# Kernel tuning notes

Hardware: AMD Instinct MI355X
Metric: run time of the kernel (lower is better)

Reference implementation:

```python
import jax, jax.numpy as jnp
import numpy as np

P = 64
K = 64
D = 2048
KERNEL_MUL = 2.0
KERNEL_NUM = 5


def setup_inputs() -> dict:
    key = jax.random.key(0)
    k1, k2 = jax.random.split(key)
    source = jax.random.normal(k1, (P * K, D), dtype=jnp.float32)
    target = jax.random.normal(k2, (P * K, D), dtype=jnp.float32)
    return {"source": source, "target": target}


def _mmd_terms(source, target):
    # split into P groups of K rows each, process all splits at once
    src = source.reshape(P, K, D)
    tgt = target.reshape(P, K, D)
    total = jnp.concatenate([src, tgt], axis=1)          # [P, 2K, D]
    n = 2 * K
    # pairwise squared L2 distances per split: [P, 2K, 2K]
    sq = jnp.sum(total * total, axis=-1)                  # [P, 2K]
    gram = jnp.einsum('pid,pjd->pij', total, total)       # [P, 2K, 2K]
    l2 = sq[:, :, None] + sq[:, None, :] - 2.0 * gram
    # bandwidth from detached distances (torch uses L2_distance.data)
    bw = jax.lax.stop_gradient(jnp.sum(l2, axis=(1, 2))) / (n * n - n)  # [P]
    bw = bw / (KERNEL_MUL ** (KERNEL_NUM // 2))
    mults = KERNEL_MUL ** jnp.arange(KERNEL_NUM, dtype=jnp.float32)     # [kn]
    bws = bw[:, None] * mults[None, :] + 1e-9                           # [P, kn]
    # multi-bandwidth Gaussian kernel sum: [P, 2K, 2K]
    kern = jnp.sum(jnp.exp(-l2[:, None, :, :] / bws[:, :, None, None]), axis=1)
    XX = kern[:, :K, :K]
    YY = kern[:, K:, K:]
    XY = kern[:, :K, K:]
    YX = kern[:, K:, :K]
    xx = jnp.mean(XX, axis=(1, 2))
    yy = jnp.mean(YY, axis=(1, 2))
    xy = jnp.mean(XY, axis=(1, 2))
    yx = jnp.mean(YX, axis=(1, 2))
    per_split_loss = xx + yy - xy - yx                    # [P]
    total_loss = jnp.sum(per_split_loss) / P
    return total_loss, l2, xx, yy, xy, yx


def reference(source, target):
    total_loss, l2, xx, yy, xy, yx = _mmd_terms(source, target)
    # original returns max of l2dist from the LAST split only
    max_l2_last = jnp.max(l2[-1])
    return (total_loss.reshape(1), max_l2_last,
            jnp.sum(xx) / P, jnp.sum(yy) / P, jnp.sum(xy) / P, jnp.sum(yx) / P)
```

## Files before the change

kernel.cpp:

```cpp
#include <hip/hip_runtime.h>

typedef _Float16 half8 __attribute__((ext_vector_type(8)));
typedef float floatx4 __attribute__((ext_vector_type(4)));
typedef unsigned int uint2v __attribute__((ext_vector_type(2)));

#define NSPLIT 64
#define KS 64
#define DIM 2048
#define NROW 128
#define BK 128
#define KSPL 4
#define KCH (DIM / KSPL)
#define NKC_A (KCH / BK)
#define SST 152
#define GSZ (NROW * NROW)
#define NBLK (NSPLIT * KSPL)
#define GT2_OFF (NBLK * GSZ)
#define PART_OFF (GT2_OFF + NBLK)


__device__ __forceinline__ unsigned int pk16(float a, float b) {
  return __builtin_bit_cast(unsigned int, __builtin_amdgcn_cvt_pkrtz(a, b));
}

__global__ __launch_bounds__(1024) void gram_kernel(const float* __restrict__ src,
                                                    const float* __restrict__ tgt,
                                                    float* __restrict__ ws) {
  __shared__ __align__(16) _Float16 stage[NROW * SST];
  __shared__ float red[16];

  const int p = blockIdx.x >> 2;
  const int c = blockIdx.x & (KSPL - 1);
  const int tid = threadIdx.x;
  const int lane = tid & 63;
  const int wave = tid >> 6;

  const int srow = tid >> 3;
  const int c4 = (tid & 7) * 4;
  const float* rowp = ((srow < KS) ? (src + (size_t)(p * KS + srow) * DIM)
                                   : (tgt + (size_t)(p * KS + (srow - KS)) * DIM)) +
                      c * KCH;

  const int wr = (wave >> 2) * 32;
  const int wc = (wave & 3) * 32;
  const int fr = lane & 15;
  const int fk = (lane >> 4) * 8;

  floatx4 acc00 = {0.f, 0.f, 0.f, 0.f};
  floatx4 acc01 = {0.f, 0.f, 0.f, 0.f};
  floatx4 acc10 = {0.f, 0.f, 0.f, 0.f};
  floatx4 acc11 = {0.f, 0.f, 0.f, 0.f};

  float4 f0, f1, f2, f3;
#define LOADK(kc)                                      \
  do {                                                 \
    const float* gp_ = rowp + (kc) * BK + c4;          \
    f0 = *(const float4*)(gp_);                        \
    f1 = *(const float4*)(gp_ + 32);                   \
    f2 = *(const float4*)(gp_ + 64);                   \
    f3 = *(const float4*)(gp_ + 96);                   \
  } while (0)

  LOADK(0);
  for (int kc = 0; kc < NKC_A; ++kc) {
    __syncthreads();
    {
      _Float16* sp = &stage[srow * SST + c4];
      *(uint2v*)(sp)      = (uint2v){pk16(f0.x, f0.y), pk16(f0.z, f0.w)};
      *(uint2v*)(sp + 32) = (uint2v){pk16(f1.x, f1.y), pk16(f1.z, f1.w)};
      *(uint2v*)(sp + 64) = (uint2v){pk16(f2.x, f2.y), pk16(f2.z, f2.w)};
      *(uint2v*)(sp + 96) = (uint2v){pk16(f3.x, f3.y), pk16(f3.z, f3.w)};
    }
    __syncthreads();
    if (kc + 1 < NKC_A) LOADK(kc + 1);
#pragma unroll
    for (int ks = 0; ks < 4; ++ks) {
      const int ko = ks * 32 + fk;
      half8 a0 = *(const half8*)&stage[(wr + fr) * SST + ko];
      half8 a1 = *(const half8*)&stage[(wr + 16 + fr) * SST + ko];
      half8 b0 = *(const half8*)&stage[(wc + fr) * SST + ko];
      half8 b1 = *(const half8*)&stage[(wc + 16 + fr) * SST + ko];
      acc00 = __builtin_amdgcn_mfma_f32_16x16x32_f16(a0, b0, acc00, 0, 0, 0);
      acc01 = __builtin_amdgcn_mfma_f32_16x16x32_f16(a0, b1, acc01, 0, 0, 0);
      acc10 = __builtin_amdgcn_mfma_f32_16x16x32_f16(a1, b0, acc10, 0, 0, 0);
      acc11 = __builtin_amdgcn_mfma_f32_16x16x32_f16(a1, b1, acc11, 0, 0, 0);
    }
  }
#undef LOADK

  float* wsp = ws + (size_t)blockIdx.x * GSZ + wave * 1024 + lane * 4;
  *(floatx4*)(wsp)       = acc00;
  *(floatx4*)(wsp + 256) = acc01;
  *(floatx4*)(wsp + 512) = acc10;
  *(floatx4*)(wsp + 768) = acc11;

  float gsum = 0.0f;
#pragma unroll
  for (int r = 0; r < 4; ++r) gsum += acc00[r] + acc01[r] + acc10[r] + acc11[r];
#pragma unroll
  for (int m = 1; m <= 32; m <<= 1) gsum += __shfl_xor(gsum, m, 64);
  if (lane == 0) red[wave] = gsum;
  __syncthreads();
  if (tid == 0) {
    float t = 0.0f;
    for (int w = 0; w < 16; ++w) t += red[w];
    ws[GT2_OFF + blockIdx.x] = t;
  }
}

__global__ __launch_bounds__(1024) void reduce_kernel(const float* __restrict__ ws,
                                                      float* __restrict__ out) {
  __shared__ float sqv[NROW];
  __shared__ float bcast[8];
  __shared__ float redm[16];
  __shared__ float quad2[2];

  const int b = blockIdx.x;
  const int p = b >> 2;
  const int rb = b & 3;
  const int tid = threadIdx.x;
  const int lane = tid & 63;
  const int wave = tid >> 6;

  const int row = rb * 32 + (tid >> 5);
  const int cg = tid & 31;

  const float* sb = ws + (size_t)(p * KSPL) * GSZ;
  const int wv = ((row >> 5) << 2) + (cg >> 3);
  const int a = (((row >> 4) & 1) << 1) + ((cg >> 2) & 1);
  const int ln = (((row & 15) >> 2) << 4) + ((cg & 3) << 2);
  const int idx = wv * 1024 + a * 256 + ln * 4 + (row & 3);

  float g0 = 0.f, g1 = 0.f, g2 = 0.f, g3 = 0.f;
#pragma unroll
  for (int c8 = 0; c8 < KSPL; ++c8) {
    const float* bp = sb + (size_t)c8 * GSZ + idx;
    g0 += bp[0]; g1 += bp[4]; g2 += bp[8]; g3 += bp[12];
  }

  if (tid < NROW) {
    const int i = tid;
    const int wd = (i >> 5) * 5;
    const int ad = ((i >> 4) & 1) * 3;
    const int lnd = (((i & 15) >> 2) << 4) + (i & 15);
    const int idxd = wd * 1024 + ad * 256 + lnd * 4 + (i & 3);
    float d = 0.0f;
#pragma unroll
    for (int c8 = 0; c8 < KSPL; ++c8) d += sb[(size_t)c8 * GSZ + idxd];
    sqv[i] = d;
  }
  if (tid < 2) quad2[tid] = 0.0f;
  __syncthreads();

  if (tid == 0) {
    float ssq = 0.0f;
    for (int i = 0; i < NROW; ++i) ssq += sqv[i];
    float gt = ws[GT2_OFF + p * 4 + 0] + ws[GT2_OFF + p * 4 + 1] +
               ws[GT2_OFF + p * 4 + 2] + ws[GT2_OFF + p * 4 + 3];
    float suml2 = 2.0f * (float)NROW * ssq - 2.0f * gt;
    float bw = suml2 / (float)(NROW * NROW - NROW) * 0.25f;
    float mult = 1.0f;
    for (int k = 0; k < 5; ++k) {
      bcast[k] = 1.0f / (bw * mult + 1e-9f);
      mult *= 2.0f;
    }
  }
  __syncthreads();

  const float sqi = sqv[row];
  float l2r[4];
  float lmax = 0.0f;
  {
    const float gg[4] = {g0, g1, g2, g3};
#pragma unroll
    for (int k = 0; k < 4; ++k) {
      float v = sqi + sqv[cg * 4 + k] - 2.0f * gg[k];
      l2r[k] = v;
      lmax = fmaxf(lmax, v);
    }
  }
#pragma unroll
  for (int m = 1; m <= 32; m <<= 1) lmax = fmaxf(lmax, __shfl_xor(lmax, m, 64));
  if (lane == 0) redm[wave] = lmax;

  const float ib0 = bcast[0], ib1 = bcast[1], ib2 = bcast[2], ib3 = bcast[3], ib4 = bcast[4];
  float qsum = 0.0f;
#pragma unroll
  for (int k = 0; k < 4; ++k) {
    float v = l2r[k];
    qsum += __expf(-v * ib0) + __expf(-v * ib1) + __expf(-v * ib2) +
            __expf(-v * ib3) + __expf(-v * ib4);
  }
  qsum += __shfl_xor(qsum, 1, 64);
  qsum += __shfl_xor(qsum, 2, 64);
  qsum += __shfl_xor(qsum, 4, 64);
  qsum += __shfl_xor(qsum, 8, 64);
  qsum += __shfl_xor(qsum, 32, 64);
  if (lane == 0) atomicAdd(&quad2[0], qsum);
  if (lane == 16) atomicAdd(&quad2[1], qsum);
  __syncthreads();

  if (tid == 0) {
    float mx = 0.0f;
    for (int w = 0; w < 16; ++w) mx = fmaxf(mx, redm[w]);
    float4* part = (float4*)(ws + PART_OFF);
    part[b] = make_float4(quad2[0], quad2[1], mx, 0.0f);
  }
}

__global__ __launch_bounds__(256) void final_kernel(const float* __restrict__ ws,
                                                    float* __restrict__ out) {
  __shared__ float fr[4][5];
  const int tid = threadIdx.x;
  const int lane = tid & 63;
  const int wave = tid >> 6;
  const float4* part = (const float4*)(ws + PART_OFF);
  float4 pt = part[tid];
  const int rb = tid & 3;
  float xx = (rb < 2) ? pt.x : 0.0f;
  float xy = (rb < 2) ? pt.y : 0.0f;
  float yx = (rb >= 2) ? pt.x : 0.0f;
  float yy = (rb >= 2) ? pt.y : 0.0f;
  float mx = ((tid >> 2) == NSPLIT - 1) ? pt.z : 0.0f;
#pragma unroll
  for (int m = 1; m <= 32; m <<= 1) {
    xx += __shfl_xor(xx, m, 64);
    xy += __shfl_xor(xy, m, 64);
    yx += __shfl_xor(yx, m, 64);
    yy += __shfl_xor(yy, m, 64);
    mx = fmaxf(mx, __shfl_xor(mx, m, 64));
  }
  if (lane == 0) {
    fr[wave][0] = xx; fr[wave][1] = xy; fr[wave][2] = yx; fr[wave][3] = yy; fr[wave][4] = mx;
  }
  __syncthreads();
  if (tid == 0) {
    float sxx = 0, sxy = 0, syx = 0, syy = 0, smx = 0;
    for (int w = 0; w < 4; ++w) {
      sxx += fr[w][0]; sxy += fr[w][1]; syx += fr[w][2]; syy += fr[w][3];
      smx = fmaxf(smx, fr[w][4]);
    }
    const float inv = 1.0f / (4096.0f * 64.0f);
    out[0] = (sxx + syy - sxy - syx) * inv;
    out[1] = smx;
    out[2] = sxx * inv;
    out[3] = syy * inv;
    out[4] = sxy * inv;
    out[5] = syx * inv;
  }
}

extern "C" void kernel_launch(void* const* d_in, const int* in_sizes, int n_in,
                              void* d_out, int out_size, void* d_ws, size_t ws_size,
                              hipStream_t stream) {
  const float* src = (const float*)d_in[0];
  const float* tgt = (const float*)d_in[1];
  float* out = (float*)d_out;
  float* ws = (float*)d_ws;
  gram_kernel<<<NBLK, 1024, 0, stream>>>(src, tgt, ws);
  reduce_kernel<<<NBLK, 1024, 0, stream>>>(ws, out);
  final_kernel<<<1, 256, 0, stream>>>(ws, out);
}
```

Baseline: 109.5 us.

## Fuse gram, reduce and final kernels into one cooperative kernel with grid syncs

Merges the three kernel launches into a single cooperative kernel that uses grid-wide syncs between the gram, per-split reduction and final reduction phases. This removes two kernel launch boundaries and their gaps. The cost is grid.sync overhead and a requirement that all 256 blocks of 1024 threads be co-resident. If they are not, the cooperative launch fails.

```diff
diff --git a/kernel.cpp b/kernel.cpp
--- a/kernel.cpp
+++ b/kernel.cpp
@@ -1,4 +1,7 @@
 #include <hip/hip_runtime.h>
+#include <hip/hip_cooperative_groups.h>
+
+namespace cg = cooperative_groups;
 
 typedef _Float16 half8 __attribute__((ext_vector_type(8)));
 typedef float floatx4 __attribute__((ext_vector_type(4)));
@@ -23,230 +26,231 @@
   return __builtin_bit_cast(unsigned int, __builtin_amdgcn_cvt_pkrtz(a, b));
 }
 
-__global__ __launch_bounds__(1024) void gram_kernel(const float* __restrict__ src,
-                                                    const float* __restrict__ tgt,
-                                                    float* __restrict__ ws) {
+__global__ __launch_bounds__(1024) void mmd_fused(const float* __restrict__ src,
+                                                  const float* __restrict__ tgt,
+                                                  float* __restrict__ ws,
+                                                  float* __restrict__ out) {
   __shared__ __align__(16) _Float16 stage[NROW * SST];
   __shared__ float red[16];
-
-  const int p = blockIdx.x >> 2;
-  const int c = blockIdx.x & (KSPL - 1);
-  const int tid = threadIdx.x;
-  const int lane = tid & 63;
-  const int wave = tid >> 6;
-
-  const int srow = tid >> 3;
-  const int c4 = (tid & 7) * 4;
-  const float* rowp = ((srow < KS) ? (src + (size_t)(p * KS + srow) * DIM)
-                                   : (tgt + (size_t)(p * KS + (srow - KS)) * DIM)) +
-                      c * KCH;
-
-  const int wr = (wave >> 2) * 32;
-  const int wc = (wave & 3) * 32;
-  const int fr = lane & 15;
-  const int fk = (lane >> 4) * 8;
-
-  floatx4 acc00 = {0.f, 0.f, 0.f, 0.f};
-  floatx4 acc01 = {0.f, 0.f, 0.f, 0.f};
-  floatx4 acc10 = {0.f, 0.f, 0.f, 0.f};
-  floatx4 acc11 = {0.f, 0.f, 0.f, 0.f};
-
-  float4 f0, f1, f2, f3;
-#define LOADK(kc)                                      \
-  do {                                                 \
-    const float* gp_ = rowp + (kc) * BK + c4;          \
-    f0 = *(const float4*)(gp_);                        \
-    f1 = *(const float4*)(gp_ + 32);                   \
-    f2 = *(const float4*)(gp_ + 64);                   \
-    f3 = *(const float4*)(gp_ + 96);                   \
-  } while (0)
-
-  LOADK(0);
-  for (int kc = 0; kc < NKC_A; ++kc) {
-    __syncthreads();
-    {
-      _Float16* sp = &stage[srow * SST + c4];
-      *(uint2v*)(sp)      = (uint2v){pk16(f0.x, f0.y), pk16(f0.z, f0.w)};
-      *(uint2v*)(sp + 32) = (uint2v){pk16(f1.x, f1.y), pk16(f1.z, f1.w)};
-      *(uint2v*)(sp + 64) = (uint2v){pk16(f2.x, f2.y), pk16(f2.z, f2.w)};
-      *(uint2v*)(sp + 96) = (uint2v){pk16(f3.x, f3.y), pk16(f3.z, f3.w)};
-    }
-    __syncthreads();
-    if (kc + 1 < NKC_A) LOADK(kc + 1);
-#pragma unroll
-    for (int ks = 0; ks < 4; ++ks) {
-      const int ko = ks * 32 + fk;
-      half8 a0 = *(const half8*)&stage[(wr + fr) * SST + ko];
-      half8 a1 = *(const half8*)&stage[(wr + 16 + fr) * SST + ko];
-      half8 b0 = *(const half8*)&stage[(wc + fr) * SST + ko];
-      half8 b1 = *(const half8*)&stage[(wc + 16 + fr) * SST + ko];
-      acc00 = __builtin_amdgcn_mfma_f32_16x16x32_f16(a0, b0, acc00, 0, 0, 0);
-      acc01 = __builtin_amdgcn_mfma_f32_16x16x32_f16(a0, b1, acc01, 0, 0, 0);
-      acc10 = __builtin_amdgcn_mfma_f32_16x16x32_f16(a1, b0, acc10, 0, 0, 0);
-      acc11 = __builtin_amdgcn_mfma_f32_16x16x32_f16(a1, b1, acc11, 0, 0, 0);
-    }
-  }
-#undef LOADK
-
-  float* wsp = ws + (size_t)blockIdx.x * GSZ + wave * 1024 + lane * 4;
-  *(floatx4*)(wsp)       = acc00;
-  *(floatx4*)(wsp + 256) = acc01;
-  *(floatx4*)(wsp + 512) = acc10;
-  *(floatx4*)(wsp + 768) = acc11;
-
-  float gsum = 0.0f;
-#pragma unroll
-  for (int r = 0; r < 4; ++r) gsum += acc00[r] + acc01[r] + acc10[r] + acc11[r];
-#pragma unroll
-  for (int m = 1; m <= 32; m <<= 1) gsum += __shfl_xor(gsum, m, 64);
-  if (lane == 0) red[wave] = gsum;
-  __syncthreads();
-  if (tid == 0) {
-    float t = 0.0f;
-    for (int w = 0; w < 16; ++w) t += red[w];
-    ws[GT2_OFF + blockIdx.x] = t;
-  }
-}
-
-__global__ __launch_bounds__(1024) void reduce_kernel(const float* __restrict__ ws,
-                                                      float* __restrict__ out) {
   __shared__ float sqv[NROW];
   __shared__ float bcast[8];
   __shared__ float redm[16];
   __shared__ float quad2[2];
+  __shared__ float fr[4][5];
+
+  cg::grid_group grid = cg::this_grid();
 
   const int b = blockIdx.x;
   const int p = b >> 2;
-  const int rb = b & 3;
+  const int c = b & (KSPL - 1);
   const int tid = threadIdx.x;
   const int lane = tid & 63;
   const int wave = tid >> 6;
 
-  const int row = rb * 32 + (tid >> 5);
-  const int cg = tid & 31;
-
-  const float* sb = ws + (size_t)(p * KSPL) * GSZ;
-  const int wv = ((row >> 5) << 2) + (cg >> 3);
-  const int a = (((row >> 4) & 1) << 1) + ((cg >> 2) & 1);
-  const int ln = (((row & 15) >> 2) << 4) + ((cg & 3) << 2);
-  const int idx = wv * 1024 + a * 256 + ln * 4 + (row & 3);
-
-  float g0 = 0.f, g1 = 0.f, g2 = 0.f, g3 = 0.f;
-#pragma unroll
-  for (int c8 = 0; c8 < KSPL; ++c8) {
-    const float* bp = sb + (size_t)c8 * GSZ + idx;
-    g0 += bp[0]; g1 += bp[4]; g2 += bp[8]; g3 += bp[12];
+  {
+    const int srow = tid >> 3;
+    const int c4 = (tid & 7) * 4;
+    const float* rowp = ((srow < KS) ? (src + (size_t)(p * KS + srow) * DIM)
+                                     : (tgt + (size_t)(p * KS + (srow - KS)) * DIM)) +
+                        c * KCH;
+
+    const int wr = (wave >> 2) * 32;
+    const int wc = (wave & 3) * 32;
+    const int frr = lane & 15;
+    const int fk = (lane >> 4) * 8;
+
+    floatx4 acc00 = {0.f, 0.f, 0.f, 0.f};
+    floatx4 acc01 = {0.f, 0.f, 0.f, 0.f};
+    floatx4 acc10 = {0.f, 0.f, 0.f, 0.f};
+    floatx4 acc11 = {0.f, 0.f, 0.f, 0.f};
+
+    float4 f0, f1, f2, f3;
+#define LOADK(kc)                                      \
+    do {                                               \
+      const float* gp_ = rowp + (kc) * BK + c4;        \
+      f0 = *(const float4*)(gp_);                      \
+      f1 = *(const float4*)(gp_ + 32);                 \
+      f2 = *(const float4*)(gp_ + 64);                 \
+      f3 = *(const float4*)(gp_ + 96);                 \
+    } while (0)
+
+    LOADK(0);
+    for (int kc = 0; kc < NKC_A; ++kc) {
+      __syncthreads();
+      {
+        _Float16* sp = &stage[srow * SST + c4];
+        *(uint2v*)(sp)      = (uint2v){pk16(f0.x, f0.y), pk16(f0.z, f0.w)};
+        *(uint2v*)(sp + 32) = (uint2v){pk16(f1.x, f1.y), pk16(f1.z, f1.w)};
+        *(uint2v*)(sp + 64) = (uint2v){pk16(f2.x, f2.y), pk16(f2.z, f2.w)};
+        *(uint2v*)(sp + 96) = (uint2v){pk16(f3.x, f3.y), pk16(f3.z, f3.w)};
+      }
+      __syncthreads();
+      if (kc + 1 < NKC_A) LOADK(kc + 1);
+#pragma unroll
+      for (int ks = 0; ks < 4; ++ks) {
+        const int ko = ks * 32 + fk;
+        half8 a0 = *(const half8*)&stage[(wr + frr) * SST + ko];
+        half8 a1 = *(const half8*)&stage[(wr + 16 + frr) * SST + ko];
+        half8 b0 = *(const half8*)&stage[(wc + frr) * SST + ko];
+        half8 b1 = *(const half8*)&stage[(wc + 16 + frr) * SST + ko];
+        acc00 = __builtin_amdgcn_mfma_f32_16x16x32_f16(a0, b0, acc00, 0, 0, 0);
+        acc01 = __builtin_amdgcn_mfma_f32_16x16x32_f16(a0, b1, acc01, 0, 0, 0);
+        acc10 = __builtin_amdgcn_mfma_f32_16x16x32_f16(a1, b0, acc10, 0, 0, 0);
+        acc11 = __builtin_amdgcn_mfma_f32_16x16x32_f16(a1, b1, acc11, 0, 0, 0);
+      }
+    }
+#undef LOADK
+
+    float* wsp = ws + (size_t)b * GSZ + wave * 1024 + lane * 4;
+    *(floatx4*)(wsp)       = acc00;
+    *(floatx4*)(wsp + 256) = acc01;
+    *(floatx4*)(wsp + 512) = acc10;
+    *(floatx4*)(wsp + 768) = acc11;
+
+    float gsum = 0.0f;
+#pragma unroll
+    for (int r = 0; r < 4; ++r) gsum += acc00[r] + acc01[r] + acc10[r] + acc11[r];
+#pragma unroll
+    for (int m = 1; m <= 32; m <<= 1) gsum += __shfl_xor(gsum, m, 64);
+    if (lane == 0) red[wave] = gsum;
+    __syncthreads();
+    if (tid == 0) {
+      float t = 0.0f;
+      for (int w = 0; w < 16; ++w) t += red[w];
+      ws[GT2_OFF + b] = t;
+    }
   }
 
-  if (tid < NROW) {
-    const int i = tid;
-    const int wd = (i >> 5) * 5;
-    const int ad = ((i >> 4) & 1) * 3;
-    const int lnd = (((i & 15) >> 2) << 4) + (i & 15);
-    const int idxd = wd * 1024 + ad * 256 + lnd * 4 + (i & 3);
-    float d = 0.0f;
-#pragma unroll
-    for (int c8 = 0; c8 < KSPL; ++c8) d += sb[(size_t)c8 * GSZ + idxd];
-    sqv[i] = d;
+  __threadfence();
+  grid.sync();
+
+  {
+    const int rb = c;
+    const int row = rb * 32 + (tid >> 5);
+    const int cg2 = tid & 31;
+
+    const float* sb = ws + (size_t)(p * KSPL) * GSZ;
+    const int wv = ((row >> 5) << 2) + (cg2 >> 3);
+    const int a = (((row >> 4) & 1) << 1) + ((cg2 >> 2) & 1);
+    const int ln = (((row & 15) >> 2) << 4) + ((cg2 & 3) << 2);
+    const int idx = wv * 1024 + a * 256 + ln * 4 + (row & 3);
+
+    float g0 = 0.f, g1 = 0.f, g2 = 0.f, g3 = 0.f;
+#pragma unroll
+    for (int c8 = 0; c8 < KSPL; ++c8) {
+      const float* bp = sb + (size_t)c8 * GSZ + idx;
+      g0 += bp[0]; g1 += bp[4]; g2 += bp[8]; g3 += bp[12];
+    }
+
+    if (tid < NROW) {
+      const int i = tid;
+      const int wd = (i >> 5) * 5;
+      const int ad = ((i >> 4) & 1) * 3;
+      const int lnd = (((i & 15) >> 2) << 4) + (i & 15);
+      const int idxd = wd * 1024 + ad * 256 + lnd * 4 + (i & 3);
+      float d = 0.0f;
+#pragma unroll
+      for (int c8 = 0; c8 < KSPL; ++c8) d += sb[(size_t)c8 * GSZ + idxd];
+      sqv[i] = d;
+    }
+    if (tid < 2) quad2[tid] = 0.0f;
+    __syncthreads();
+
+    if (tid == 0) {
+      float ssq = 0.0f;
+      for (int i = 0; i < NROW; ++i) ssq += sqv[i];
+      float gt = ws[GT2_OFF + p * 4 + 0] + ws[GT2_OFF + p * 4 + 1] +
+                 ws[GT2_OFF + p * 4 + 2] + ws[GT2_OFF + p * 4 + 3];
+      float suml2 = 2.0f * (float)NROW * ssq - 2.0f * gt;
+      float bwv = suml2 / (float)(NROW * NROW - NROW) * 0.25f;
+      float mult = 1.0f;
+      for (int k = 0; k < 5; ++k) {
+        bcast[k] = 1.0f / (bwv * mult + 1e-9f);
+        mult *= 2.0f;
+      }
+    }
+    __syncthreads();
+
+    const float sqi = sqv[row];
+    float l2r[4];
+    float lmax = 0.0f;
+    {
+      const float gg[4] = {g0, g1, g2, g3};
+#pragma unroll
+      for (int k = 0; k < 4; ++k) {
+        float v = sqi + sqv[cg2 * 4 + k] - 2.0f * gg[k];
+        l2r[k] = v;
+        lmax = fmaxf(lmax, v);
+      }
+    }
+#pragma unroll
+    for (int m = 1; m <= 32; m <<= 1) lmax = fmaxf(lmax, __shfl_xor(lmax, m, 64));
+    if (lane == 0) redm[wave] = lmax;
+
+    const float ib0 = bcast[0], ib1 = bcast[1], ib2 = bcast[2], ib3 = bcast[3], ib4 = bcast[4];
+    float qsum = 0.0f;
+#pragma unroll
+    for (int k = 0; k < 4; ++k) {
+      float v = l2r[k];
+      qsum += __expf(-v * ib0) + __expf(-v * ib1) + __expf(-v * ib2) +
+              __expf(-v * ib3) + __expf(-v * ib4);
+    }
+    qsum += __shfl_xor(qsum, 1, 64);
+    qsum += __shfl_xor(qsum, 2, 64);
+    qsum += __shfl_xor(qsum, 4, 64);
+    qsum += __shfl_xor(qsum, 8, 64);
+    qsum += __shfl_xor(qsum, 32, 64);
+    if (lane == 0) atomicAdd(&quad2[0], qsum);
+    if (lane == 16) atomicAdd(&quad2[1], qsum);
+    __syncthreads();
+
+    if (tid == 0) {
+      float mx = 0.0f;
+      for (int w = 0; w < 16; ++w) mx = fmaxf(mx, redm[w]);
+      float4* part = (float4*)(ws + PART_OFF);
+      part[b] = make_float4(quad2[0], quad2[1], mx, 0.0f);
+    }
   }
-  if (tid < 2) quad2[tid] = 0.0f;
-  __syncthreads();
-
-  if (tid == 0) {
-    float ssq = 0.0f;
-    for (int i = 0; i < NROW; ++i) ssq += sqv[i];
-    float gt = ws[GT2_OFF + p * 4 + 0] + ws[GT2_OFF + p * 4 + 1] +
-               ws[GT2_OFF + p * 4 + 2] + ws[GT2_OFF + p * 4 + 3];
-    float suml2 = 2.0f * (float)NROW * ssq - 2.0f * gt;
-    float bw = suml2 / (float)(NROW * NROW - NROW) * 0.25f;
-    float mult = 1.0f;
-    for (int k = 0; k < 5; ++k) {
-      bcast[k] = 1.0f / (bw * mult + 1e-9f);
-      mult *= 2.0f;
-    }
-  }
-  __syncthreads();
-
-  const float sqi = sqv[row];
-  float l2r[4];
-  float lmax = 0.0f;
-  {
-    const float gg[4] = {g0, g1, g2, g3};
-#pragma unroll
-    for (int k = 0; k < 4; ++k) {
-      float v = sqi + sqv[cg * 4 + k] - 2.0f * gg[k];
-      l2r[k] = v;
-      lmax = fmaxf(lmax, v);
-    }
-  }
-#pragma unroll
-  for (int m = 1; m <= 32; m <<= 1) lmax = fmaxf(lmax, __shfl_xor(lmax, m, 64));
-  if (lane == 0) redm[wave] = lmax;
-
-  const float ib0 = bcast[0], ib1 = bcast[1], ib2 = bcast[2], ib3 = bcast[3], ib4 = bcast[4];
-  float qsum = 0.0f;
-#pragma unroll
-  for (int k = 0; k < 4; ++k) {
-    float v = l2r[k];
-    qsum += __expf(-v * ib0) + __expf(-v * ib1) + __expf(-v * ib2) +
-            __expf(-v * ib3) + __expf(-v * ib4);
-  }
-  qsum += __shfl_xor(qsum, 1, 64);
-  qsum += __shfl_xor(qsum, 2, 64);
-  qsum += __shfl_xor(qsum, 4, 64);
-  qsum += __shfl_xor(qsum, 8, 64);
-  qsum += __shfl_xor(qsum, 32, 64);
-  if (lane == 0) atomicAdd(&quad2[0], qsum);
-  if (lane == 16) atomicAdd(&quad2[1], qsum);
-  __syncthreads();
-
-  if (tid == 0) {
-    float mx = 0.0f;
-    for (int w = 0; w < 16; ++w) mx = fmaxf(mx, redm[w]);
-    float4* part = (float4*)(ws + PART_OFF);
-    part[b] = make_float4(quad2[0], quad2[1], mx, 0.0f);
-  }
-}
-
-__global__ __launch_bounds__(256) void final_kernel(const float* __restrict__ ws,
-                                                    float* __restrict__ out) {
-  __shared__ float fr[4][5];
-  const int tid = threadIdx.x;
-  const int lane = tid & 63;
-  const int wave = tid >> 6;
-  const float4* part = (const float4*)(ws + PART_OFF);
-  float4 pt = part[tid];
-  const int rb = tid & 3;
-  float xx = (rb < 2) ? pt.x : 0.0f;
-  float xy = (rb < 2) ? pt.y : 0.0f;
-  float yx = (rb >= 2) ? pt.x : 0.0f;
-  float yy = (rb >= 2) ? pt.y : 0.0f;
-  float mx = ((tid >> 2) == NSPLIT - 1) ? pt.z : 0.0f;
-#pragma unroll
-  for (int m = 1; m <= 32; m <<= 1) {
-    xx += __shfl_xor(xx, m, 64);
-    xy += __shfl_xor(xy, m, 64);
-    yx += __shfl_xor(yx, m, 64);
-    yy += __shfl_xor(yy, m, 64);
-    mx = fmaxf(mx, __shfl_xor(mx, m, 64));
-  }
-  if (lane == 0) {
-    fr[wave][0] = xx; fr[wave][1] = xy; fr[wave][2] = yx; fr[wave][3] = yy; fr[wave][4] = mx;
-  }
-  __syncthreads();
-  if (tid == 0) {
-    float sxx = 0, sxy = 0, syx = 0, syy = 0, smx = 0;
-    for (int w = 0; w < 4; ++w) {
-      sxx += fr[w][0]; sxy += fr[w][1]; syx += fr[w][2]; syy += fr[w][3];
-      smx = fmaxf(smx, fr[w][4]);
-    }
-    const float inv = 1.0f / (4096.0f * 64.0f);
-    out[0] = (sxx + syy - sxy - syx) * inv;
-    out[1] = smx;
-    out[2] = sxx * inv;
-    out[3] = syy * inv;
-    out[4] = sxy * inv;
-    out[5] = syx * inv;
+
+  __threadfence();
+  grid.sync();
+
+  if (b == 0) {
+    float xx = 0.f, xy = 0.f, yx = 0.f, yy = 0.f, mx = 0.f;
+    if (tid < NBLK) {
+      const float4* part = (const float4*)(ws + PART_OFF);
+      float4 pt = part[tid];
+      int rbq = tid & 3;
+      if (rbq < 2) { xx = pt.x; xy = pt.y; }
+      else         { yx = pt.x; yy = pt.y; }
+      if ((tid >> 2) == NSPLIT - 1) mx = pt.z;
+    }
+#pragma unroll
+    for (int m = 1; m <= 32; m <<= 1) {
+      xx += __shfl_xor(xx, m, 64);
+      xy += __shfl_xor(xy, m, 64);
+      yx += __shfl_xor(yx, m, 64);
+      yy += __shfl_xor(yy, m, 64);
+      mx = fmaxf(mx, __shfl_xor(mx, m, 64));
+    }
+    if (lane == 0 && wave < 4) {
+      fr[wave][0] = xx; fr[wave][1] = xy; fr[wave][2] = yx; fr[wave][3] = yy; fr[wave][4] = mx;
+    }
+    __syncthreads();
+    if (tid == 0) {
+      float sxx = 0, sxy = 0, syx = 0, syy = 0, smx = 0;
+      for (int w = 0; w < 4; ++w) {
+        sxx += fr[w][0]; sxy += fr[w][1]; syx += fr[w][2]; syy += fr[w][3];
+        smx = fmaxf(smx, fr[w][4]);
+      }
+      const float inv = 1.0f / (4096.0f * 64.0f);
+      out[0] = (sxx + syy - sxy - syx) * inv;
+      out[1] = smx;
+      out[2] = sxx * inv;
+      out[3] = syy * inv;
+      out[4] = sxy * inv;
+      out[5] = syx * inv;
+    }
   }
 }
 
@@ -257,7 +261,7 @@
   const float* tgt = (const float*)d_in[1];
   float* out = (float*)d_out;
   float* ws = (float*)d_ws;
-  gram_kernel<<<NBLK, 1024, 0, stream>>>(src, tgt, ws);
-  reduce_kernel<<<NBLK, 1024, 0, stream>>>(ws, out);
-  final_kernel<<<1, 256, 0, stream>>>(ws, out);
+  void* args[] = {(void*)&src, (void*)&tgt, (void*)&ws, (void*)&out};
+  hipLaunchCooperativeKernel((const void*)mmd_fused, dim3(NBLK), dim3(1024), args, 0,
+                             stream);
 }
```

Result: slower. 304.5 us (+178.2%).

## Store partial Gram tiles as fp16 and fuse final reduction via last-block atomic

Applied to the files above, without the earlier changes.

The gram kernel now writes its partial Gram tiles to the workspace in fp16 rather than fp32, halving the intermediate traffic between kernels. The final single-block kernel is removed. Its reduction now runs inside reduce_kernel, in whichever block is last to increment a global atomic counter. That counter is zeroed by a memset before launch. The changes save a kernel launch and intermediate bandwidth, but add an extra memset node and fp16 rounding of partial Gram sums, whose values can be large (around D) and therefore lose precision in the distances.

```diff
diff --git a/kernel.cpp b/kernel.cpp
--- a/kernel.cpp
+++ b/kernel.cpp
@@ -1,6 +1,7 @@
 #include <hip/hip_runtime.h>
 
 typedef _Float16 half8 __attribute__((ext_vector_type(8)));
+typedef _Float16 half4v __attribute__((ext_vector_type(4)));
 typedef float floatx4 __attribute__((ext_vector_type(4)));
 typedef unsigned int uint2v __attribute__((ext_vector_type(2)));
 
@@ -15,8 +16,9 @@
 #define SST 152
 #define GSZ (NROW * NROW)
 #define NBLK (NSPLIT * KSPL)
-#define GT2_OFF (NBLK * GSZ)
-#define PART_OFF (GT2_OFF + NBLK)
+#define GT2F_OFF (NBLK * GSZ / 2)
+#define PART_OFF (GT2F_OFF + NBLK)
+#define FLAG_OFF (PART_OFF + NBLK * 4)
 
 
 __device__ __forceinline__ unsigned int pk16(float a, float b) {
@@ -88,11 +90,21 @@
   }
 #undef LOADK
 
-  float* wsp = ws + (size_t)blockIdx.x * GSZ + wave * 1024 + lane * 4;
-  *(floatx4*)(wsp)       = acc00;
-  *(floatx4*)(wsp + 256) = acc01;
-  *(floatx4*)(wsp + 512) = acc10;
-  *(floatx4*)(wsp + 768) = acc11;
+  _Float16* hs = (_Float16*)ws + (size_t)blockIdx.x * GSZ + wave * 1024 + lane * 4;
+  {
+    half4v h0, h1, h2, h3;
+#pragma unroll
+    for (int r = 0; r < 4; ++r) {
+      h0[r] = (_Float16)acc00[r];
+      h1[r] = (_Float16)acc01[r];
+      h2[r] = (_Float16)acc10[r];
+      h3[r] = (_Float16)acc11[r];
+    }
+    *(half4v*)(hs)       = h0;
+    *(half4v*)(hs + 256) = h1;
+    *(half4v*)(hs + 512) = h2;
+    *(half4v*)(hs + 768) = h3;
+  }
 
   float gsum = 0.0f;
 #pragma unroll
@@ -104,16 +116,18 @@
   if (tid == 0) {
     float t = 0.0f;
     for (int w = 0; w < 16; ++w) t += red[w];
-    ws[GT2_OFF + blockIdx.x] = t;
-  }
-}
-
-__global__ __launch_bounds__(1024) void reduce_kernel(const float* __restrict__ ws,
+    ws[GT2F_OFF + blockIdx.x] = t;
+  }
+}
+
+__global__ __launch_bounds__(1024) void reduce_kernel(float* __restrict__ ws,
                                                       float* __restrict__ out) {
   __shared__ float sqv[NROW];
   __shared__ float bcast[8];
   __shared__ float redm[16];
   __shared__ float quad2[2];
+  __shared__ float fr2[4][5];
+  __shared__ int sh_go;
 
   const int b = blockIdx.x;
   const int p = b >> 2;
@@ -121,11 +135,12 @@
   const int tid = threadIdx.x;
   const int lane = tid & 63;
   const int wave = tid >> 6;
+  int* iflag = (int*)(ws + FLAG_OFF);
 
   const int row = rb * 32 + (tid >> 5);
   const int cg = tid & 31;
 
-  const float* sb = ws + (size_t)(p * KSPL) * GSZ;
+  const _Float16* sb = (const _Float16*)ws + (size_t)(p * KSPL) * GSZ;
   const int wv = ((row >> 5) << 2) + (cg >> 3);
   const int a = (((row >> 4) & 1) << 1) + ((cg >> 2) & 1);
   const int ln = (((row & 15) >> 2) << 4) + ((cg & 3) << 2);
@@ -134,8 +149,8 @@
   float g0 = 0.f, g1 = 0.f, g2 = 0.f, g3 = 0.f;
 #pragma unroll
   for (int c8 = 0; c8 < KSPL; ++c8) {
-    const float* bp = sb + (size_t)c8 * GSZ + idx;
-    g0 += bp[0]; g1 += bp[4]; g2 += bp[8]; g3 += bp[12];
+    const _Float16* bp = sb + (size_t)c8 * GSZ + idx;
+    g0 += (float)bp[0]; g1 += (float)bp[4]; g2 += (float)bp[8]; g3 += (float)bp[12];
   }
 
   if (tid < NROW) {
@@ -146,7 +161,7 @@
     const int idxd = wd * 1024 + ad * 256 + lnd * 4 + (i & 3);
     float d = 0.0f;
 #pragma unroll
-    for (int c8 = 0; c8 < KSPL; ++c8) d += sb[(size_t)c8 * GSZ + idxd];
+    for (int c8 = 0; c8 < KSPL; ++c8) d += (float)sb[(size_t)c8 * GSZ + idxd];
     sqv[i] = d;
   }
   if (tid < 2) quad2[tid] = 0.0f;
@@ -155,8 +170,8 @@
   if (tid == 0) {
     float ssq = 0.0f;
     for (int i = 0; i < NROW; ++i) ssq += sqv[i];
-    float gt = ws[GT2_OFF + p * 4 + 0] + ws[GT2_OFF + p * 4 + 1] +
-               ws[GT2_OFF + p * 4 + 2] + ws[GT2_OFF + p * 4 + 3];
+    float gt = ws[GT2F_OFF + p * 4 + 0] + ws[GT2F_OFF + p * 4 + 1] +
+               ws[GT2F_OFF + p * 4 + 2] + ws[GT2F_OFF + p * 4 + 3];
     float suml2 = 2.0f * (float)NROW * ssq - 2.0f * gt;
     float bw = suml2 / (float)(NROW * NROW - NROW) * 0.25f;
     float mult = 1.0f;
@@ -206,22 +221,25 @@
     float4* part = (float4*)(ws + PART_OFF);
     part[b] = make_float4(quad2[0], quad2[1], mx, 0.0f);
   }
-}
-
-__global__ __launch_bounds__(256) void final_kernel(const float* __restrict__ ws,
-                                                    float* __restrict__ out) {
-  __shared__ float fr[4][5];
-  const int tid = threadIdx.x;
-  const int lane = tid & 63;
-  const int wave = tid >> 6;
-  const float4* part = (const float4*)(ws + PART_OFF);
-  float4 pt = part[tid];
-  const int rb = tid & 3;
-  float xx = (rb < 2) ? pt.x : 0.0f;
-  float xy = (rb < 2) ? pt.y : 0.0f;
-  float yx = (rb >= 2) ? pt.x : 0.0f;
-  float yy = (rb >= 2) ? pt.y : 0.0f;
-  float mx = ((tid >> 2) == NSPLIT - 1) ? pt.z : 0.0f;
+
+  __syncthreads();
+  if (tid == 0) {
+    int prev = __hip_atomic_fetch_add(&iflag[0], 1, __ATOMIC_ACQ_REL,
+                                      __HIP_MEMORY_SCOPE_AGENT);
+    sh_go = (prev == NBLK - 1) ? 1 : 0;
+  }
+  __syncthreads();
+  if (!sh_go) return;
+
+  float xx = 0.f, xy = 0.f, yx = 0.f, yy = 0.f, mx = 0.f;
+  if (tid < NBLK) {
+    const float4* part = (const float4*)(ws + PART_OFF);
+    float4 pt = part[tid];
+    int rbq = tid & 3;
+    if (rbq < 2) { xx = pt.x; xy = pt.y; }
+    else         { yx = pt.x; yy = pt.y; }
+    if ((tid >> 2) == NSPLIT - 1) mx = pt.z;
+  }
 #pragma unroll
   for (int m = 1; m <= 32; m <<= 1) {
     xx += __shfl_xor(xx, m, 64);
@@ -230,15 +248,15 @@
     yy += __shfl_xor(yy, m, 64);
     mx = fmaxf(mx, __shfl_xor(mx, m, 64));
   }
-  if (lane == 0) {
-    fr[wave][0] = xx; fr[wave][1] = xy; fr[wave][2] = yx; fr[wave][3] = yy; fr[wave][4] = mx;
+  if (lane == 0 && wave < 4) {
+    fr2[wave][0] = xx; fr2[wave][1] = xy; fr2[wave][2] = yx; fr2[wave][3] = yy; fr2[wave][4] = mx;
   }
   __syncthreads();
   if (tid == 0) {
     float sxx = 0, sxy = 0, syx = 0, syy = 0, smx = 0;
     for (int w = 0; w < 4; ++w) {
-      sxx += fr[w][0]; sxy += fr[w][1]; syx += fr[w][2]; syy += fr[w][3];
-      smx = fmaxf(smx, fr[w][4]);
+      sxx += fr2[w][0]; sxy += fr2[w][1]; syx += fr2[w][2]; syy += fr2[w][3];
+      smx = fmaxf(smx, fr2[w][4]);
     }
     const float inv = 1.0f / (4096.0f * 64.0f);
     out[0] = (sxx + syy - sxy - syx) * inv;
@@ -257,7 +275,7 @@
   const float* tgt = (const float*)d_in[1];
   float* out = (float*)d_out;
   float* ws = (float*)d_ws;
+  hipMemsetAsync(ws + FLAG_OFF, 0, sizeof(int), stream);
   gram_kernel<<<NBLK, 1024, 0, stream>>>(src, tgt, ws);
   reduce_kernel<<<NBLK, 1024, 0, stream>>>(ws, out);
-  final_kernel<<<1, 256, 0, stream>>>(ws, out);
-}
+}
```

Measured after the change: 112.5 us. 2.8% more time.
